# Kernel tuning notes

Measured on AMD Instinct MI355X. Metric: run time of the kernel, lower is better.

## Reference

```python
import jax, jax.numpy as jnp
import numpy as np

NUM_HEADS = 16

def _alibi(S, H, dtype):
    # fairseq-style ALiBi: slopes[h] * -(|i-j|), H assumed power of 2
    start = 2.0 ** (-8.0 / H)
    slopes = start ** jnp.arange(1, H + 1, dtype=jnp.float32)      # [H]
    pos = jnp.arange(S)
    rel = -jnp.abs(pos[None, :] - pos[:, None]).astype(jnp.float32)  # [S,S]
    return (slopes[:, None, None] * rel).astype(dtype)             # [H,S,S]

def setup_inputs() -> dict:
    key = jax.random.key(0)
    kx, km, kw1, kw2 = jax.random.split(key, 4)
    B, S, D = 2, 2048, 1024
    inputs = jax.random.normal(kx, (B, S, D), dtype=jnp.float32)
    mask = jax.random.bernoulli(km, 0.9, (B, S))
    mask = mask.at[:, 0].set(True)  # ensure each row has a valid key
    Wqkv = jax.random.normal(kw1, (3 * D, D), dtype=jnp.float32) * 0.02
    bqkv = jnp.zeros((3 * D,), dtype=jnp.float32)
    Wproj = jax.random.normal(kw2, (D, D), dtype=jnp.float32) * 0.02
    bproj = jnp.zeros((D,), dtype=jnp.float32)
    return {"inputs": inputs, "mask": mask, "Wqkv": Wqkv, "bqkv": bqkv,
            "Wproj": Wproj, "bproj": bproj}

def reference(inputs, mask, Wqkv, bqkv, Wproj, bproj):
    B, S, D = inputs.shape
    H = NUM_HEADS
    dh = D // H
    scale = D ** (-0.5)  # NOTE: original scales by full dim, not head dim
    qkv = inputs @ Wqkv.T + bqkv                       # [B,S,3D]
    qkv = qkv.reshape(B, S, H, 3 * dh).transpose(0, 2, 1, 3)  # [B,H,S,3dh]
    q, k, v = qkv[..., :dh], qkv[..., dh:2 * dh], qkv[..., 2 * dh:]
    attn = jnp.einsum('bhqd,bhkd->bhqk', q, k) * scale  # [B,H,S,S]
    attn = attn + _alibi(S, H, attn.dtype)[None]
    attn = jnp.where(mask[:, None, None, :], attn, jnp.finfo(attn.dtype).min)
    attn = jax.nn.softmax(attn, axis=-1)
    x = jnp.einsum('bhqk,bhkd->bhqd', attn, v)          # [B,H,S,dh]
    x = x.transpose(0, 2, 1, 3).reshape(B, S, D)
    return x @ Wproj.T + bproj
```

## Files before the change

### kernel.cpp

```cpp
#include <hip/hip_runtime.h>
#include <cstdint>
#include <cstddef>

#define B_  2
#define S_  2048
#define D_  1024
#define H_  16
#define DH_ 64
#define M_  (B_*S_)
#define N3_ (3*D_)
#define NT_ (S_/64)

typedef float f32x4 __attribute__((ext_vector_type(4)));
typedef short short8 __attribute__((ext_vector_type(8)));
typedef unsigned short u16x8 __attribute__((ext_vector_type(8)));
typedef unsigned short u16x4 __attribute__((ext_vector_type(4)));
typedef unsigned short u16x2 __attribute__((ext_vector_type(2)));

__device__ __forceinline__ unsigned short f2bf(float x) {
    unsigned int u = __float_as_uint(x);
    unsigned int r = (u + 0x7FFFu + ((u >> 16) & 1u)) >> 16;
    return (unsigned short)r;
}

__device__ __forceinline__ float exp2_(float x) { return __builtin_amdgcn_exp2f(x); }

__device__ __forceinline__ unsigned int cvt_pk_bf16(float a, float b) {
    unsigned int r;
    asm volatile("v_cvt_pk_bf16_f32 %0, %1, %2" : "=v"(r) : "v"(a), "v"(b));
    return r;
}

__device__ __forceinline__ int xcd_swizzle(int lin, int nwg) {
    const int cpx = nwg >> 3;
    return (lin & 7) * cpx + (lin >> 3);
}

__device__ __forceinline__ void gload16(const void* g, void* l) {
    __builtin_amdgcn_global_load_lds(
        (const __attribute__((address_space(1))) unsigned int*)g,
        (__attribute__((address_space(3))) unsigned int*)l,
        16, 0, 0);
}

__global__ void k_detect_mask(const unsigned char* __restrict__ mb, int* __restrict__ flag) {
    __shared__ int sBig, sM4, sM8;
    if (threadIdx.x == 0) { sBig = 0; sM4 = 0; sM8 = 0; }
    __syncthreads();
    int big = 0, m4 = 0, m8 = 0;
    for (int i = threadIdx.x; i < 4096; i += blockDim.x) {
        unsigned char v = mb[i];
        if (v > 1) big = 1;
        if (v && (i & 3)) m4 = 1;
        if (v && ((i & 7) == 4)) m8 = 1;
    }
    if (big) atomicOr(&sBig, 1);
    if (m4)  atomicOr(&sM4, 1);
    if (m8)  atomicOr(&sM8, 1);
    __syncthreads();
    if (threadIdx.x == 0) {
        int w;
        if (sBig)      w = 0;
        else if (sM4)  w = 1;
        else if (sM8)  w = 4;
        else           w = 8;
        *flag = w;
    }
}

__global__ void k_expand_mask(const void* __restrict__ mask, const int* __restrict__ flag,
                              float* __restrict__ maskbias, int n) {
    int i = blockIdx.x * blockDim.x + threadIdx.x;
    if (i >= n) return;
    int w = *flag;
    bool on;
    if (w == 0)      on = ((const float*)mask)[i] != 0.0f;
    else if (w == 1) on = ((const unsigned char*)mask)[i] != 0;
    else if (w == 4) on = ((const int*)mask)[i] != 0;
    else             on = ((const long long*)mask)[i] != 0;
    maskbias[i] = on ? 0.0f : -1e30f;
}

__global__ void k_f2bf3(const float* __restrict__ A, const float* __restrict__ B2,
                        const float* __restrict__ C, unsigned short* __restrict__ oA,
                        unsigned short* __restrict__ oB, unsigned short* __restrict__ oC) {
    const int nA = M_ * D_, nB = N3_ * D_, nC = D_ * D_;
    int i = (blockIdx.x * 256 + threadIdx.x) * 4;
    const float* src; unsigned short* dst; int off;
    if (i < nA)           { src = A;  dst = oA; off = i; }
    else if (i < nA + nB) { src = B2; dst = oB; off = i - nA; }
    else if (i < nA + nB + nC) { src = C; dst = oC; off = i - nA - nB; }
    else return;
    float4 v = *reinterpret_cast<const float4*>(&src[off]);
    u16x4 o = { f2bf(v.x), f2bf(v.y), f2bf(v.z), f2bf(v.w) };
    *reinterpret_cast<u16x4*>(&dst[off]) = o;
}

template <bool OUT_BF16>
__global__ __launch_bounds__(512) void k_gemm_bf16_cv(
    const unsigned short* __restrict__ A, const unsigned short* __restrict__ W,
    const float* __restrict__ bias, void* __restrict__ Cout,
    int M, int N, int K) {
    __shared__ __align__(16) unsigned short Al[3][128 * 64];
    __shared__ __align__(16) unsigned short Wl[3][128 * 64];

    const int tid  = threadIdx.x;
    const int lane = tid & 63;
    const int w    = tid >> 6;
    const int wr   = w >> 2, wc = w & 3;
    const int l16  = lane & 15, g = lane >> 4;
    const int m0 = blockIdx.y * 128, n0 = blockIdx.x * 128;
    const int NTk = K >> 6;

    f32x4 acc[4][2];
#pragma unroll
    for (int m = 0; m < 4; ++m)
#pragma unroll
        for (int n = 0; n < 2; ++n) acc[m][n] = (f32x4){0.f, 0.f, 0.f, 0.f};

    auto issueTile = [&](int kt) {
        const int k0 = kt << 6;
        unsigned short* Ad = Al[kt % 3];
        unsigned short* Wd = Wl[kt % 3];
#pragma unroll
        for (int i = 0; i < 2; ++i) {
            const int c = i * 512 + tid;
            const int row = c >> 3;
            const int colel = (((c & 7) ^ (row & 7)) << 3);
            gload16(A + (size_t)(m0 + row) * K + k0 + colel, Ad + c * 8);
            gload16(W + (size_t)(n0 + row) * K + k0 + colel, Wd + c * 8);
        }
    };

    issueTile(0);
    issueTile(1);

    for (int t = 0; t < NTk; ++t) {
        if (t + 2 < NTk) issueTile(t + 2);

        if (t < NTk - 2)       asm volatile("s_waitcnt vmcnt(8)" ::: "memory");
        else if (t == NTk - 2) asm volatile("s_waitcnt vmcnt(4)" ::: "memory");
        else                   asm volatile("s_waitcnt vmcnt(0)" ::: "memory");
        __builtin_amdgcn_s_barrier();
        __builtin_amdgcn_sched_barrier(0);

        const unsigned short* Ab = Al[t % 3];
        const unsigned short* Wb = Wl[t % 3];
        short8 a[4][2], b[2][2];
#pragma unroll
        for (int m = 0; m < 4; ++m)
#pragma unroll
            for (int kk = 0; kk < 2; ++kk) {
                const int row = wr * 64 + m * 16 + l16;
                const int kb = (kk * 64 + g * 16) ^ ((row & 7) << 4);
                a[m][kk] = *reinterpret_cast<const short8*>(
                    (const char*)Ab + row * 128 + kb);
            }
#pragma unroll
        for (int n = 0; n < 2; ++n)
#pragma unroll
            for (int kk = 0; kk < 2; ++kk) {
                const int row = wc * 32 + n * 16 + l16;
                const int kb = (kk * 64 + g * 16) ^ ((row & 7) << 4);
                b[n][kk] = *reinterpret_cast<const short8*>(
                    (const char*)Wb + row * 128 + kb);
            }

        __builtin_amdgcn_s_setprio(1);
#pragma unroll
        for (int kk = 0; kk < 2; ++kk)
#pragma unroll
            for (int m = 0; m < 4; ++m)
#pragma unroll
                for (int n = 0; n < 2; ++n)
                    acc[m][n] = __builtin_amdgcn_mfma_f32_16x16x32_bf16(
                        a[m][kk], b[n][kk], acc[m][n], 0, 0, 0);
        __builtin_amdgcn_s_setprio(0);

        __builtin_amdgcn_sched_barrier(0);
        __builtin_amdgcn_s_barrier();
    }

    float bv[2];
#pragma unroll
    for (int n = 0; n < 2; ++n) bv[n] = bias[n0 + wc * 32 + n * 16 + l16];
#pragma unroll
    for (int m = 0; m < 4; ++m) {
#pragma unroll
        for (int r = 0; r < 4; ++r) {
            const size_t row = m0 + wr * 64 + m * 16 + g * 4 + r;
#pragma unroll
            for (int n = 0; n < 2; ++n) {
                const int col = n0 + wc * 32 + n * 16 + l16;
                float v = acc[m][n][r] + bv[n];
                if (OUT_BF16)
                    ((unsigned short*)Cout)[row * N + col] = f2bf(v);
                else
                    ((float*)Cout)[row * N + col] = v;
            }
        }
    }
}

__global__ __launch_bounds__(512, 4) void k_attn_mfma(
    const unsigned short* __restrict__ qkv,
    const float* __restrict__ maskbias,
    unsigned short* __restrict__ x) {
    __shared__ __align__(16) unsigned short Kt[2][64][72];
    __shared__ __align__(16) unsigned short Vt[3][64][72];
    __shared__ __align__(16) unsigned short QP[128][72];

    const int tid  = threadIdx.x;
    const int lane = tid & 63;
    const int wq   = tid >> 6;
    const int g    = lane >> 4;
    const int g4   = g * 4;
    const int l16  = lane & 15;

    const int nqt = S_ / 128;
    const int nwg = B_ * H_ * nqt;
    const int bid = xcd_swizzle(blockIdx.x, nwg);
    const int qt = bid % nqt;
    const int h  = (bid / nqt) % H_;
    const int b  = bid / (nqt * H_);
    const int q0 = qt * 128;
    const size_t rowbase = (size_t)b * S_ * N3_;
    const int hq = h * 192, hk = hq + 64, hv = hq + 128;
    const unsigned short* kvb = qkv + rowbase;
    const float* mbp = maskbias + b * S_;

    {
        const int row = tid >> 2, cb = (tid & 3) * 16;
        const unsigned short* src = kvb + (size_t)(q0 + row) * N3_ + hq + cb;
        *reinterpret_cast<u16x8*>(&QP[row][cb])     = *reinterpret_cast<const u16x8*>(src);
        *reinterpret_cast<u16x8*>(&QP[row][cb + 8]) = *reinterpret_cast<const u16x8*>(src + 8);
    }

    const int krow = tid >> 3, kcb = (tid & 7) * 8;
    const int vkb = (tid & 31) * 2, vdb = (tid >> 5) * 4;
    u16x8 kr;
    u16x4 vr0, vr1;

    {
        kr  = *reinterpret_cast<const u16x8*>(kvb + (size_t)krow * N3_ + hk + kcb);
        const unsigned short* vs = kvb + (size_t)vkb * N3_ + hv + vdb;
        vr0 = *reinterpret_cast<const u16x4*>(vs);
        vr1 = *reinterpret_cast<const u16x4*>(vs + N3_);
        *reinterpret_cast<u16x8*>(&Kt[0][krow][kcb]) = kr;
#pragma unroll
        for (int j = 0; j < 4; ++j)
            *reinterpret_cast<u16x2*>(&Vt[0][vdb + j][vkb]) = (u16x2){vr0[j], vr1[j]};
    }
    __syncthreads();

    const short8 qa0 = *reinterpret_cast<const short8*>(&QP[wq*16 + l16][g*8]);
    const short8 qa1 = *reinterpret_cast<const short8*>(&QP[wq*16 + l16][32 + g*8]);

    f32x4 Oacc[4];
#pragma unroll
    for (int df = 0; df < 4; ++df) Oacc[df] = (f32x4){0.f, 0.f, 0.f, 0.f};
    float m = -1e30f, l = 0.0f;

    const float LOG2E = 1.4426950408889634f;
    const float c1 = 0.03125f * LOG2E;
    const float c2 = exp2f(-0.5f * (float)(h + 1)) * LOG2E;
    const int   qw0 = q0 + wq * 16;
    const int   qg  = qw0 + l16;
    float albr[4];
#pragma unroll
    for (int r = 0; r < 4; ++r) albr[r] = c2 * (float)(g4 + r);
    const float c2_16 = c2 * 16.0f;

    float p_[4][4];

    {
        kr  = *reinterpret_cast<const u16x8*>(kvb + (size_t)(64 + krow) * N3_ + hk + kcb);
        const unsigned short* vs = kvb + (size_t)(64 + vkb) * N3_ + hv + vdb;
        vr0 = *reinterpret_cast<const u16x4*>(vs);
        vr1 = *reinterpret_cast<const u16x4*>(vs + N3_);

        __builtin_amdgcn_s_setprio(1);
#pragma unroll
        for (int jb = 0; jb < 4; ++jb) {
            short8 kb0 = *reinterpret_cast<const short8*>(&Kt[0][jb*16 + l16][g*8]);
            short8 kb1 = *reinterpret_cast<const short8*>(&Kt[0][jb*16 + l16][32 + g*8]);
            f32x4 c = (f32x4){0.f, 0.f, 0.f, 0.f};
            c = __builtin_amdgcn_mfma_f32_16x16x32_bf16(kb0, qa0, c, 0, 0, 0);
            c = __builtin_amdgcn_mfma_f32_16x16x32_bf16(kb1, qa1, c, 0, 0, 0);
#pragma unroll
            for (int r = 0; r < 4; ++r) p_[jb][r] = c[r];
        }
        __builtin_amdgcn_s_setprio(0);

        *reinterpret_cast<u16x8*>(&Kt[1][krow][kcb]) = kr;
#pragma unroll
        for (int j = 0; j < 4; ++j)
            *reinterpret_cast<u16x2*>(&Vt[1][vdb + j][vkb]) = (u16x2){vr0[j], vr1[j]};
    }
    __syncthreads();
    {
        kr  = *reinterpret_cast<const u16x8*>(kvb + (size_t)(128 + krow) * N3_ + hk + kcb);
        const unsigned short* vs = kvb + (size_t)(128 + vkb) * N3_ + hv + vdb;
        vr0 = *reinterpret_cast<const u16x4*>(vs);
        vr1 = *reinterpret_cast<const u16x4*>(vs + N3_);
    }

    int vb_r = 0;
    int vb_w = 2;

    for (int t = 1; t < NT_ + 1; ++t) {
        const int k0m = (t - 1) * 64;

        f32x4 amv[4];
#pragma unroll
        for (int jb = 0; jb < 4; ++jb)
            amv[jb] = *reinterpret_cast<const f32x4*>(&mbp[k0m + jb * 16 + g4]);

        f32x4 cnx[4];
        if (t < NT_) {
            const unsigned short (*Kc)[72] = Kt[t & 1];
            __builtin_amdgcn_s_setprio(1);
#pragma unroll
            for (int jb = 0; jb < 4; ++jb) {
                short8 kb0 = *reinterpret_cast<const short8*>(&Kc[jb*16 + l16][g*8]);
                short8 kb1 = *reinterpret_cast<const short8*>(&Kc[jb*16 + l16][32 + g*8]);
                f32x4 c = (f32x4){0.f, 0.f, 0.f, 0.f};
                c = __builtin_amdgcn_mfma_f32_16x16x32_bf16(kb0, qa0, c, 0, 0, 0);
                c = __builtin_amdgcn_mfma_f32_16x16x32_bf16(kb1, qa1, c, 0, 0, 0);
                cnx[jb] = c;
            }
            __builtin_amdgcn_s_setprio(0);
        }

        if (k0m + 64 <= qw0) {
            const float tb = c2 * (float)(k0m - qg);
#pragma unroll
            for (int jb = 0; jb < 4; ++jb) {
                const float tbj = tb + c2_16 * (float)jb;
#pragma unroll
                for (int r = 0; r < 4; ++r)
                    p_[jb][r] = fmaf(p_[jb][r], c1, tbj + albr[r] + amv[jb][r]);
            }
        } else if (k0m >= qw0 + 16) {
            const float tb = c2 * (float)(k0m - qg);
#pragma unroll
            for (int jb = 0; jb < 4; ++jb) {
                const float tbj = -tb - c2_16 * (float)jb;
#pragma unroll
                for (int r = 0; r < 4; ++r)
                    p_[jb][r] = fmaf(p_[jb][r], c1, tbj - albr[r] + amv[jb][r]);
            }
        } else {
            const int dbase = k0m - qg;
#pragma unroll
            for (int jb = 0; jb < 4; ++jb)
#pragma unroll
                for (int r = 0; r < 4; ++r) {
                    int d = dbase + jb * 16 + g4 + r;
                    d = d < 0 ? -d : d;
                    p_[jb][r] = fmaf(p_[jb][r], c1, amv[jb][r] - c2 * (float)d);
                }
        }

        float mx;
        {
            float m0_ = fmaxf(fmaxf(p_[0][0], p_[0][1]), fmaxf(p_[0][2], p_[0][3]));
            float m1_ = fmaxf(fmaxf(p_[1][0], p_[1][1]), fmaxf(p_[1][2], p_[1][3]));
            float m2_ = fmaxf(fmaxf(p_[2][0], p_[2][1]), fmaxf(p_[2][2], p_[2][3]));
            float m3_ = fmaxf(fmaxf(p_[3][0], p_[3][1]), fmaxf(p_[3][2], p_[3][3]));
            mx = fmaxf(fmaxf(m0_, m1_), fmaxf(m2_, m3_));
        }
        mx = fmaxf(mx, __shfl_xor(mx, 16));
        mx = fmaxf(mx, __shfl_xor(mx, 32));

        if (__any(mx > m + 8.0f)) {
            const float mn = fmaxf(m, mx);
            const float cr = exp2_(m - mn);
            m = mn;
            l *= cr;
            const int srcb = (lane & 48) + ((lane & 48) >> 2);
#pragma unroll
            for (int r = 0; r < 4; ++r) {
                const float crq = __shfl(cr, srcb + r);
#pragma unroll
                for (int df = 0; df < 4; ++df) Oacc[df][r] *= crq;
            }
        }

        float ps = 0.0f;
#pragma unroll
        for (int jb = 0; jb < 4; ++jb)
#pragma unroll
            for (int r = 0; r < 4; ++r) {
                float p = exp2_(p_[jb][r] - m);
                p_[jb][r] = p;
                ps += p;
            }

#pragma unroll
        for (int jb = 0; jb < 4; ++jb) {
            uint2 st;
            st.x = cvt_pk_bf16(p_[jb][0], p_[jb][1]);
            st.y = cvt_pk_bf16(p_[jb][2], p_[jb][3]);
            *reinterpret_cast<uint2*>(&QP[wq*16 + l16][jb*16 + g4]) = st;
        }

        {
            const short8 pa0 = *reinterpret_cast<const short8*>(&QP[wq*16 + l16][g*8]);
            const short8 pa1 = *reinterpret_cast<const short8*>(&QP[wq*16 + l16][32 + g*8]);
            const unsigned short (*Vc)[72] = Vt[vb_r];
            __builtin_amdgcn_s_setprio(1);
#pragma unroll
            for (int df = 0; df < 4; ++df) {
                short8 vb0 = *reinterpret_cast<const short8*>(&Vc[df*16 + l16][g*8]);
                short8 vb1 = *reinterpret_cast<const short8*>(&Vc[df*16 + l16][32 + g*8]);
                Oacc[df] = __builtin_amdgcn_mfma_f32_16x16x32_bf16(pa0, vb0, Oacc[df], 0, 0, 0);
                Oacc[df] = __builtin_amdgcn_mfma_f32_16x16x32_bf16(pa1, vb1, Oacc[df], 0, 0, 0);
            }
            __builtin_amdgcn_s_setprio(0);
        }

        ps += __shfl_xor(ps, 16);
        ps += __shfl_xor(ps, 32);
        l += ps;

        if (t + 1 < NT_) {
            *reinterpret_cast<u16x8*>(&Kt[(t + 1) & 1][krow][kcb]) = kr;
#pragma unroll
            for (int j = 0; j < 4; ++j)
                *reinterpret_cast<u16x2*>(&Vt[vb_w][vdb + j][vkb]) = (u16x2){vr0[j], vr1[j]};
            __syncthreads();
            if (t + 2 < NT_) {
                const int kn = (t + 2) * 64;
                kr  = *reinterpret_cast<const u16x8*>(kvb + (size_t)(kn + krow) * N3_ + hk + kcb);
                const unsigned short* vs = kvb + (size_t)(kn + vkb) * N3_ + hv + vdb;
                vr0 = *reinterpret_cast<const u16x4*>(vs);
                vr1 = *reinterpret_cast<const u16x4*>(vs + N3_);
            }
        }
        vb_r = (vb_r == 2) ? 0 : vb_r + 1;
        vb_w = (vb_w == 2) ? 0 : vb_w + 1;

        if (t < NT_) {
#pragma unroll
            for (int jb = 0; jb < 4; ++jb)
#pragma unroll
                for (int r = 0; r < 4; ++r) p_[jb][r] = cnx[jb][r];
        }
    }

    const int srcb = (lane & 48) + ((lane & 48) >> 2);
    float invq[4];
#pragma unroll
    for (int r = 0; r < 4; ++r) invq[r] = 1.0f / __shfl(l, srcb + r);
#pragma unroll
    for (int df = 0; df < 4; ++df) {
#pragma unroll
        for (int r = 0; r < 4; ++r) {
            const int qrow = q0 + wq * 16 + g4 + r;
            x[(size_t)(b * S_ + qrow) * D_ + h * 64 + df * 16 + l16] = f2bf(Oacc[df][r] * invq[r]);
        }
    }
}

extern "C" void kernel_launch(void* const* d_in, const int* in_sizes, int n_in,
                              void* d_out, int out_size, void* d_ws, size_t ws_size,
                              hipStream_t stream) {
    const float* inputs = (const float*)d_in[0];
    const void*  mask   = d_in[1];
    const float* Wqkv   = (const float*)d_in[2];
    const float* bqkv   = (const float*)d_in[3];
    const float* Wproj  = (const float*)d_in[4];
    const float* bproj  = (const float*)d_in[5];
    float* out = (float*)d_out;

    unsigned short* qkvb = (unsigned short*)d_ws;
    unsigned short* xb   = qkvb + (size_t)M_ * N3_;
    unsigned short* Ab   = xb + (size_t)M_ * D_;
    unsigned short* Wqb  = Ab + (size_t)M_ * D_;
    unsigned short* Wpb  = Wqb + (size_t)N3_ * D_;
    float* maskbias = (float*)(Wpb + (size_t)D_ * D_);
    int*   flag     = (int*)(maskbias + M_);

    k_detect_mask<<<1, 256, 0, stream>>>((const unsigned char*)mask, flag);
    k_expand_mask<<<(M_ + 255) / 256, 256, 0, stream>>>(mask, flag, maskbias, M_);

    const int ntot = M_ * D_ + N3_ * D_ + D_ * D_;
    k_f2bf3<<<(ntot / 4 + 255) / 256, 256, 0, stream>>>(inputs, Wqkv, Wproj, Ab, Wqb, Wpb);

    dim3 g1(N3_ / 128, M_ / 128);
    k_gemm_bf16_cv<true><<<g1, 512, 0, stream>>>(Ab, Wqb, bqkv, qkvb, M_, N3_, D_);

    k_attn_mfma<<<B_ * H_ * (S_ / 128), 512, 0, stream>>>(qkvb, maskbias, xb);

    dim3 g2(D_ / 128, M_ / 128);
    k_gemm_bf16_cv<false><<<g2, 512, 0, stream>>>(xb, Wpb, bproj, out, M_, D_, D_);
}
```

Baseline: 166.0 us.

## Keep softmax P in registers via permuted key rows; fuse mask kernels

The attention kernel permutes which K rows each lane computes, so the QK^T MFMA output lands directly in the A-operand layout of the PV MFMA. This lets P be packed to bf16 in registers instead of taking a round trip through the LDS QP buffer. Q is loaded straight from global memory, and the LDS row padding changes from 72 to 76. The ALiBi and mask offsets are rewritten for the new key ordering, and the two mask kernels are merged into one launch, at the cost of every block redoing the dtype detection.

```diff
diff --git a/kernel.cpp b/kernel.cpp
--- a/kernel.cpp
+++ b/kernel.cpp
@@ -13,6 +13,7 @@
 
 typedef float f32x4 __attribute__((ext_vector_type(4)));
 typedef short short8 __attribute__((ext_vector_type(8)));
+typedef int   i32x4 __attribute__((ext_vector_type(4)));
 typedef unsigned short u16x8 __attribute__((ext_vector_type(8)));
 typedef unsigned short u16x4 __attribute__((ext_vector_type(4)));
 typedef unsigned short u16x2 __attribute__((ext_vector_type(2)));
@@ -43,12 +44,12 @@
         16, 0, 0);
 }
 
-__global__ void k_detect_mask(const unsigned char* __restrict__ mb, int* __restrict__ flag) {
+__global__ void k_mask(const unsigned char* __restrict__ mb, float* __restrict__ maskbias) {
     __shared__ int sBig, sM4, sM8;
     if (threadIdx.x == 0) { sBig = 0; sM4 = 0; sM8 = 0; }
     __syncthreads();
     int big = 0, m4 = 0, m8 = 0;
-    for (int i = threadIdx.x; i < 4096; i += blockDim.x) {
+    for (int i = threadIdx.x; i < 4096; i += 256) {
         unsigned char v = mb[i];
         if (v > 1) big = 1;
         if (v && (i & 3)) m4 = 1;
@@ -58,26 +59,13 @@
     if (m4)  atomicOr(&sM4, 1);
     if (m8)  atomicOr(&sM8, 1);
     __syncthreads();
-    if (threadIdx.x == 0) {
-        int w;
-        if (sBig)      w = 0;
-        else if (sM4)  w = 1;
-        else if (sM8)  w = 4;
-        else           w = 8;
-        *flag = w;
-    }
-}
-
-__global__ void k_expand_mask(const void* __restrict__ mask, const int* __restrict__ flag,
-                              float* __restrict__ maskbias, int n) {
-    int i = blockIdx.x * blockDim.x + threadIdx.x;
-    if (i >= n) return;
-    int w = *flag;
+    const int w = sBig ? 0 : (sM4 ? 1 : (sM8 ? 4 : 8));
+    const int i = blockIdx.x * 256 + threadIdx.x;
     bool on;
-    if (w == 0)      on = ((const float*)mask)[i] != 0.0f;
-    else if (w == 1) on = ((const unsigned char*)mask)[i] != 0;
-    else if (w == 4) on = ((const int*)mask)[i] != 0;
-    else             on = ((const long long*)mask)[i] != 0;
+    if (w == 0)      on = ((const float*)mb)[i] != 0.0f;
+    else if (w == 1) on = mb[i] != 0;
+    else if (w == 4) on = ((const int*)mb)[i] != 0;
+    else             on = ((const long long*)mb)[i] != 0;
     maskbias[i] = on ? 0.0f : -1e30f;
 }
 
@@ -206,9 +194,8 @@
     const unsigned short* __restrict__ qkv,
     const float* __restrict__ maskbias,
     unsigned short* __restrict__ x) {
-    __shared__ __align__(16) unsigned short Kt[2][64][72];
-    __shared__ __align__(16) unsigned short Vt[3][64][72];
-    __shared__ __align__(16) unsigned short QP[128][72];
+    __shared__ __align__(16) unsigned short Kt[2][64][76];
+    __shared__ __align__(16) unsigned short Vt[3][64][76];
 
     const int tid  = threadIdx.x;
     const int lane = tid & 63;
@@ -229,12 +216,11 @@
     const unsigned short* kvb = qkv + rowbase;
     const float* mbp = maskbias + b * S_;
 
-    {
-        const int row = tid >> 2, cb = (tid & 3) * 16;
-        const unsigned short* src = kvb + (size_t)(q0 + row) * N3_ + hq + cb;
-        *reinterpret_cast<u16x8*>(&QP[row][cb])     = *reinterpret_cast<const u16x8*>(src);
-        *reinterpret_cast<u16x8*>(&QP[row][cb + 8]) = *reinterpret_cast<const u16x8*>(src + 8);
-    }
+    const int blrow = 8 * (l16 >> 2) + (l16 & 3);
+
+    const unsigned short* qrp = kvb + (size_t)(q0 + wq * 16 + l16) * N3_ + hq;
+    const short8 qa0 = *reinterpret_cast<const short8*>(qrp + g * 8);
+    const short8 qa1 = *reinterpret_cast<const short8*>(qrp + 32 + g * 8);
 
     const int krow = tid >> 3, kcb = (tid & 7) * 8;
     const int vkb = (tid & 31) * 2, vdb = (tid >> 5) * 4;
@@ -253,9 +239,6 @@
     }
     __syncthreads();
 
-    const short8 qa0 = *reinterpret_cast<const short8*>(&QP[wq*16 + l16][g*8]);
-    const short8 qa1 = *reinterpret_cast<const short8*>(&QP[wq*16 + l16][32 + g*8]);
-
     f32x4 Oacc[4];
 #pragma unroll
     for (int df = 0; df < 4; ++df) Oacc[df] = (f32x4){0.f, 0.f, 0.f, 0.f};
@@ -266,10 +249,12 @@
     const float c2 = exp2f(-0.5f * (float)(h + 1)) * LOG2E;
     const int   qw0 = q0 + wq * 16;
     const int   qg  = qw0 + l16;
+    const float alg = c2 * (float)(8 * g);
     float albr[4];
 #pragma unroll
-    for (int r = 0; r < 4; ++r) albr[r] = c2 * (float)(g4 + r);
-    const float c2_16 = c2 * 16.0f;
+    for (int r = 0; r < 4; ++r) albr[r] = c2 * (float)r;
+    const float ckb[4] = { 0.0f, c2 * 4.0f, c2 * 32.0f, c2 * 36.0f };
+    const int   KBJ[4] = { 0, 4, 32, 36 };
 
     float p_[4][4];
 
@@ -282,8 +267,9 @@
         __builtin_amdgcn_s_setprio(1);
 #pragma unroll
         for (int jb = 0; jb < 4; ++jb) {
-            short8 kb0 = *reinterpret_cast<const short8*>(&Kt[0][jb*16 + l16][g*8]);
-            short8 kb1 = *reinterpret_cast<const short8*>(&Kt[0][jb*16 + l16][32 + g*8]);
+            const int rw = blrow + KBJ[jb];
+            short8 kb0 = *reinterpret_cast<const short8*>(&Kt[0][rw][g*8]);
+            short8 kb1 = *reinterpret_cast<const short8*>(&Kt[0][rw][32 + g*8]);
             f32x4 c = (f32x4){0.f, 0.f, 0.f, 0.f};
             c = __builtin_amdgcn_mfma_f32_16x16x32_bf16(kb0, qa0, c, 0, 0, 0);
             c = __builtin_amdgcn_mfma_f32_16x16x32_bf16(kb1, qa1, c, 0, 0, 0);
@@ -314,16 +300,17 @@
         f32x4 amv[4];
 #pragma unroll
         for (int jb = 0; jb < 4; ++jb)
-            amv[jb] = *reinterpret_cast<const f32x4*>(&mbp[k0m + jb * 16 + g4]);
+            amv[jb] = *reinterpret_cast<const f32x4*>(&mbp[k0m + 8 * g + KBJ[jb]]);
 
         f32x4 cnx[4];
         if (t < NT_) {
-            const unsigned short (*Kc)[72] = Kt[t & 1];
+            const unsigned short (*Kc)[76] = Kt[t & 1];
             __builtin_amdgcn_s_setprio(1);
 #pragma unroll
             for (int jb = 0; jb < 4; ++jb) {
-                short8 kb0 = *reinterpret_cast<const short8*>(&Kc[jb*16 + l16][g*8]);
-                short8 kb1 = *reinterpret_cast<const short8*>(&Kc[jb*16 + l16][32 + g*8]);
+                const int rw = blrow + KBJ[jb];
+                short8 kb0 = *reinterpret_cast<const short8*>(&Kc[rw][g*8]);
+                short8 kb1 = *reinterpret_cast<const short8*>(&Kc[rw][32 + g*8]);
                 f32x4 c = (f32x4){0.f, 0.f, 0.f, 0.f};
                 c = __builtin_amdgcn_mfma_f32_16x16x32_bf16(kb0, qa0, c, 0, 0, 0);
                 c = __builtin_amdgcn_mfma_f32_16x16x32_bf16(kb1, qa1, c, 0, 0, 0);
@@ -333,30 +320,30 @@
         }
 
         if (k0m + 64 <= qw0) {
-            const float tb = c2 * (float)(k0m - qg);
+            const float tbg = c2 * (float)(k0m - qg) + alg;
 #pragma unroll
             for (int jb = 0; jb < 4; ++jb) {
-                const float tbj = tb + c2_16 * (float)jb;
+                const float tbj = tbg + ckb[jb];
 #pragma unroll
                 for (int r = 0; r < 4; ++r)
                     p_[jb][r] = fmaf(p_[jb][r], c1, tbj + albr[r] + amv[jb][r]);
             }
         } else if (k0m >= qw0 + 16) {
-            const float tb = c2 * (float)(k0m - qg);
+            const float tbg = c2 * (float)(k0m - qg) + alg;
 #pragma unroll
             for (int jb = 0; jb < 4; ++jb) {
-                const float tbj = -tb - c2_16 * (float)jb;
+                const float tbj = -tbg - ckb[jb];
 #pragma unroll
                 for (int r = 0; r < 4; ++r)
                     p_[jb][r] = fmaf(p_[jb][r], c1, tbj - albr[r] + amv[jb][r]);
             }
         } else {
-            const int dbase = k0m - qg;
+            const int dbase = k0m - qg + 8 * g;
 #pragma unroll
             for (int jb = 0; jb < 4; ++jb)
 #pragma unroll
                 for (int r = 0; r < 4; ++r) {
-                    int d = dbase + jb * 16 + g4 + r;
+                    int d = dbase + KBJ[jb] + r;
                     d = d < 0 ? -d : d;
                     p_[jb][r] = fmaf(p_[jb][r], c1, amv[jb][r] - c2 * (float)d);
                 }
@@ -397,18 +384,22 @@
                 ps += p;
             }
 
-#pragma unroll
-        for (int jb = 0; jb < 4; ++jb) {
-            uint2 st;
-            st.x = cvt_pk_bf16(p_[jb][0], p_[jb][1]);
-            st.y = cvt_pk_bf16(p_[jb][2], p_[jb][3]);
-            *reinterpret_cast<uint2*>(&QP[wq*16 + l16][jb*16 + g4]) = st;
-        }
-
+        short8 pa0, pa1;
         {
-            const short8 pa0 = *reinterpret_cast<const short8*>(&QP[wq*16 + l16][g*8]);
-            const short8 pa1 = *reinterpret_cast<const short8*>(&QP[wq*16 + l16][32 + g*8]);
-            const unsigned short (*Vc)[72] = Vt[vb_r];
+            i32x4 w0 = { (int)cvt_pk_bf16(p_[0][0], p_[0][1]),
+                         (int)cvt_pk_bf16(p_[0][2], p_[0][3]),
+                         (int)cvt_pk_bf16(p_[1][0], p_[1][1]),
+                         (int)cvt_pk_bf16(p_[1][2], p_[1][3]) };
+            i32x4 w1 = { (int)cvt_pk_bf16(p_[2][0], p_[2][1]),
+                         (int)cvt_pk_bf16(p_[2][2], p_[2][3]),
+                         (int)cvt_pk_bf16(p_[3][0], p_[3][1]),
+                         (int)cvt_pk_bf16(p_[3][2], p_[3][3]) };
+            pa0 = __builtin_bit_cast(short8, w0);
+            pa1 = __builtin_bit_cast(short8, w1);
+        }
+
+        {
+            const unsigned short (*Vc)[76] = Vt[vb_r];
             __builtin_amdgcn_s_setprio(1);
 #pragma unroll
             for (int df = 0; df < 4; ++df) {
@@ -480,10 +471,8 @@
     unsigned short* Wqb  = Ab + (size_t)M_ * D_;
     unsigned short* Wpb  = Wqb + (size_t)N3_ * D_;
     float* maskbias = (float*)(Wpb + (size_t)D_ * D_);
-    int*   flag     = (int*)(maskbias + M_);
-
-    k_detect_mask<<<1, 256, 0, stream>>>((const unsigned char*)mask, flag);
-    k_expand_mask<<<(M_ + 255) / 256, 256, 0, stream>>>(mask, flag, maskbias, M_);
+
+    k_mask<<<M_ / 256, 256, 0, stream>>>((const unsigned char*)mask, maskbias);
 
     const int ntot = M_ * D_ + N3_ * D_ + D_ * D_;
     k_f2bf3<<<(ntot / 4 + 255) / 256, 256, 0, stream>>>(inputs, Wqkv, Wproj, Ab, Wqb, Wpb);
```

After: 336.9 us. 103% more time.
